# Kernel optimization log

Hardware: AMD Instinct MI355X
Metric: run time of the kernel (lower is better)

Reference implementation:

```python
import jax, jax.numpy as jnp
import numpy as np

B, S, E, H, NE, K = 4, 1024, 1024, 16, 8, 2
DFF = 4 * E
DH = E // H
EPS = 1e-5


def _ln(x, g, b):
    m = jnp.mean(x, axis=-1, keepdims=True)
    v = jnp.mean(jnp.square(x - m), axis=-1, keepdims=True)
    return (x - m) * jax.lax.rsqrt(v + EPS) * g + b


def setup_inputs() -> dict:
    key = jax.random.key(0)
    ks = jax.random.split(key, 20)
    n = lambda k, sh, s: (jax.random.normal(k, sh, jnp.float32) * s)
    return {
        'x': n(ks[0], (B, S, E), 1.0),
        'ln1_g': jnp.ones((E,), jnp.float32), 'ln1_b': jnp.zeros((E,), jnp.float32),
        'wq': n(ks[1], (E, E), 0.02), 'bq': jnp.zeros((E,), jnp.float32),
        'wk': n(ks[2], (E, E), 0.02), 'bk': jnp.zeros((E,), jnp.float32),
        'wv': n(ks[3], (E, E), 0.02), 'bv': jnp.zeros((E,), jnp.float32),
        'wo': n(ks[4], (E, E), 0.02), 'bo': jnp.zeros((E,), jnp.float32),
        'ln2_g': jnp.ones((E,), jnp.float32), 'ln2_b': jnp.zeros((E,), jnp.float32),
        'sw1': n(ks[5], (E, DFF), 0.02), 'sb1': jnp.zeros((DFF,), jnp.float32),
        'sw2': n(ks[6], (DFF, E), 0.02), 'sb2': jnp.zeros((E,), jnp.float32),
        'ew1': n(ks[7], (NE, E, DFF), 0.02), 'eb1': jnp.zeros((NE, DFF), jnp.float32),
        'ew2': n(ks[8], (NE, DFF, E), 0.02), 'eb2': jnp.zeros((NE, E), jnp.float32),
        'w_gate': n(ks[9], (E, NE), 1.0),
    }


def reference(x, ln1_g, ln1_b, wq, bq, wk, bk, wv, bv, wo, bo,
              ln2_g, ln2_b, sw1, sb1, sw2, sb2, ew1, eb1, ew2, eb2, w_gate):
    # --- self-attention sublayer (eval: no dropout) ---
    res1 = x
    h = _ln(x, ln1_g, ln1_b)
    q = (h @ wq + bq).reshape(B, S, H, DH)
    k = (h @ wk + bk).reshape(B, S, H, DH)
    v = (h @ wv + bv).reshape(B, S, H, DH)
    scores = jnp.einsum('bqhd,bkhd->bhqk', q, k) / jnp.sqrt(jnp.float32(DH))
    attn = jax.nn.softmax(scores, axis=-1)
    ctx = jnp.einsum('bhqk,bkhd->bqhd', attn, v).reshape(B, S, E)
    x = res1 + (ctx @ wo + bo)

    # --- MoE sublayer ---
    res2 = x
    h2 = _ln(x, ln2_g, ln2_b)
    shared = jax.nn.gelu(h2 @ sw1 + sb1, approximate=False) @ sw2 + sb2

    # router (eval: clean logits, no noise)
    logits = h2 @ w_gate                                  # (B,S,NE)
    top_vals, top_idx = jax.lax.top_k(logits, K)          # (B,S,K)
    top_gates = jax.nn.softmax(top_vals, axis=-1)
    onehot = jax.nn.one_hot(top_idx, NE, dtype=x.dtype)   # (B,S,K,NE)
    gates = jnp.einsum('bsk,bske->bse', top_gates, onehot)
    probs = jax.nn.softmax(logits, axis=-1).reshape(-1, NE)
    P = probs.mean(0)
    f = (gates > 0).astype(x.dtype).reshape(-1, NE).mean(0)
    aux_loss = NE * jnp.sum(P * f)

    # dense all-expert compute, gated combine (matches original math)
    eh = jax.nn.gelu(jnp.einsum('bse,neh->bnsh', h2, ew1) + eb1[None, :, None, :],
                     approximate=False)
    eo = jnp.einsum('bnsh,nhe->bnse', eh, ew2) + eb2[None, :, None, :]
    expert_out = jnp.einsum('bnse,bsn->bse', eo, gates)

    return res2 + shared + expert_out, aux_loss
```

## Files before the change

kernel.cpp:

```cpp
#include <hip/hip_runtime.h>
#include <stdint.h>

#define B_    4
#define S_    1024
#define E_    1024
#define H_    16
#define NE_   8
#define DFF_  4096
#define NT_   4096
#define QS_   3072
#define ROWCAP_ 9216

typedef unsigned short u16;
typedef short bf16x8 __attribute__((ext_vector_type(8)));
typedef float f32x4 __attribute__((ext_vector_type(4)));

__device__ __forceinline__ float bf2f(u16 u){ unsigned v = ((unsigned)u) << 16; return __builtin_bit_cast(float, v); }
__device__ __forceinline__ u16 f2bf(float f){ unsigned x = __builtin_bit_cast(unsigned, f); return (u16)((x + 0x7FFFu + ((x >> 16) & 1u)) >> 16); }
__device__ __forceinline__ float gelu_f(float x){ return 0.5f * x * (1.f + erff(x * 0.70710678118f)); }

__device__ __forceinline__ void gl_lds16(const u16* g, u16* l){
  __builtin_amdgcn_global_load_lds((__attribute__((address_space(1))) void*)(const_cast<u16*>(g)),
                                   (__attribute__((address_space(3))) void*)(l), 16, 0, 0);
}

__launch_bounds__(256)
__global__ void ln_kernel(const float* __restrict__ x, const float* __restrict__ g,
                          const float* __restrict__ be, u16* __restrict__ out)
{
  const int row = blockIdx.x;
  const float4 v = ((const float4*)(x + (size_t)row * E_))[threadIdx.x];
  float s = v.x + v.y + v.z + v.w;
  #pragma unroll
  for(int mm = 32; mm >= 1; mm >>= 1) s += __shfl_xor(s, mm);
  __shared__ float red[8];
  const int wid = threadIdx.x >> 6;
  if((threadIdx.x & 63) == 0) red[wid] = s;
  __syncthreads();
  const float mean = (red[0] + red[1] + red[2] + red[3]) * (1.0f / E_);
  const float d0 = v.x - mean, d1 = v.y - mean, d2 = v.z - mean, d3 = v.w - mean;
  float q2 = d0*d0 + d1*d1 + d2*d2 + d3*d3;
  #pragma unroll
  for(int mm = 32; mm >= 1; mm >>= 1) q2 += __shfl_xor(q2, mm);
  if((threadIdx.x & 63) == 0) red[4 + wid] = q2;
  __syncthreads();
  const float var = (red[4] + red[5] + red[6] + red[7]) * (1.0f / E_);
  const float rs = rsqrtf(var + 1e-5f);
  const float4 gg = ((const float4*)g)[threadIdx.x];
  const float4 bb = ((const float4*)be)[threadIdx.x];
  ushort4 o;
  o.x = f2bf(d0 * rs * gg.x + bb.x);
  o.y = f2bf(d1 * rs * gg.y + bb.y);
  o.z = f2bf(d2 * rs * gg.z + bb.z);
  o.w = f2bf(d3 * rs * gg.w + bb.w);
  ((ushort4*)(out + (size_t)row * E_))[threadIdx.x] = o;
}

__launch_bounds__(256)
__global__ void transpose_kernel(const float* __restrict__ W, u16* __restrict__ WT, int K, int N)
{
  __shared__ __align__(16) u16 t[64][72];
  const size_t zo = (size_t)blockIdx.z * K * N;
  const int k0 = blockIdx.x * 64, n0 = blockIdx.y * 64;
  const int tid = threadIdx.x;
  const int kr = tid >> 2;
  const int nc = (tid & 3) * 4;
  #pragma unroll
  for(int p = 0; p < 4; p++){
    float4 v = *(const float4*)(W + zo + (size_t)(k0 + kr) * N + n0 + nc + p * 16);
    t[nc + p*16 + 0][kr] = f2bf(v.x);
    t[nc + p*16 + 1][kr] = f2bf(v.y);
    t[nc + p*16 + 2][kr] = f2bf(v.z);
    t[nc + p*16 + 3][kr] = f2bf(v.w);
  }
  __syncthreads();
  const int nr = tid >> 3;
  const int kg = (tid & 7) * 8;
  #pragma unroll
  for(int p = 0; p < 2; p++){
    const int nn = nr + p * 32;
    unsigned u0 = t[nn][kg+0], u1 = t[nn][kg+1], u2 = t[nn][kg+2], u3 = t[nn][kg+3];
    unsigned u4 = t[nn][kg+4], u5 = t[nn][kg+5], u6 = t[nn][kg+6], u7 = t[nn][kg+7];
    uint4 o;
    o.x = u0 | (u1 << 16); o.y = u2 | (u3 << 16); o.z = u4 | (u5 << 16); o.w = u6 | (u7 << 16);
    *(uint4*)(WT + zo + (size_t)(n0 + nn) * K + k0 + kg) = o;
  }
}

__global__ void bcat_kernel(const float* __restrict__ bq, const float* __restrict__ bk,
                            const float* __restrict__ bv, float* __restrict__ bcat)
{
  const int i = blockIdx.x * 256 + threadIdx.x;
  if(i < 1024) bcat[i] = bq[i];
  else if(i < 2048) bcat[i] = bk[i - 1024];
  else if(i < 3072) bcat[i] = bv[i - 2048];
}

template<int MODE>
__launch_bounds__(256)
__global__ void gemm_kernel(const u16* __restrict__ A, const u16* __restrict__ Bt,
                            int N, int Kd, const float* __restrict__ bias,
                            u16* __restrict__ outB)
{
  __shared__ __align__(16) u16 As0[4096], Bs0[4096], As1[4096], Bs1[4096];
  const int tid = threadIdx.x, lane = tid & 63, wid = tid >> 6;
  const int wm = wid >> 1, wn = wid & 1;
  const int tm = blockIdx.y * 128, tn = blockIdx.x * 128;

  const f32x4 zero = {0.f, 0.f, 0.f, 0.f};
  f32x4 acc[4][4];
  #pragma unroll
  for(int m = 0; m < 4; m++)
    #pragma unroll
    for(int n = 0; n < 4; n++) acc[m][n] = zero;

  const u16* gA0 = A  + (size_t)(tm + wid*32 + (lane >> 2)) * Kd + ((lane & 3) << 3);
  const u16* gA1 = gA0 + (size_t)16 * Kd;
  const u16* gB0 = Bt + (size_t)(tn + wid*32 + (lane >> 2)) * Kd + ((lane & 3) << 3);
  const u16* gB1 = gB0 + (size_t)16 * Kd;
  u16* lA0 = As0 + wid*1024; u16* lA1 = lA0 + 512;
  u16* lB0 = Bs0 + wid*1024; u16* lB1 = lB0 + 512;
  u16* lA0b = As1 + wid*1024; u16* lA1b = lA0b + 512;
  u16* lB0b = Bs1 + wid*1024; u16* lB1b = lB0b + 512;

  for(int k0 = 0; k0 < Kd; k0 += 64){
    __syncthreads();
    gl_lds16(gA0 + k0, lA0);  gl_lds16(gA1 + k0, lA1);
    gl_lds16(gB0 + k0, lB0);  gl_lds16(gB1 + k0, lB1);
    gl_lds16(gA0 + k0+32, lA0b); gl_lds16(gA1 + k0+32, lA1b);
    gl_lds16(gB0 + k0+32, lB0b); gl_lds16(gB1 + k0+32, lB1b);
    __syncthreads();
    bf16x8 aF[4], bF[4];
    #pragma unroll
    for(int m = 0; m < 4; m++) aF[m] = *(const bf16x8*)(As0 + (wm*64 + m*16 + (lane & 15)) * 32 + ((lane >> 4) << 3));
    #pragma unroll
    for(int n = 0; n < 4; n++) bF[n] = *(const bf16x8*)(Bs0 + (wn*64 + n*16 + (lane & 15)) * 32 + ((lane >> 4) << 3));
    #pragma unroll
    for(int m = 0; m < 4; m++)
      #pragma unroll
      for(int n = 0; n < 4; n++)
        acc[m][n] = __builtin_amdgcn_mfma_f32_16x16x32_bf16(aF[m], bF[n], acc[m][n], 0, 0, 0);
    #pragma unroll
    for(int m = 0; m < 4; m++) aF[m] = *(const bf16x8*)(As1 + (wm*64 + m*16 + (lane & 15)) * 32 + ((lane >> 4) << 3));
    #pragma unroll
    for(int n = 0; n < 4; n++) bF[n] = *(const bf16x8*)(Bs1 + (wn*64 + n*16 + (lane & 15)) * 32 + ((lane >> 4) << 3));
    #pragma unroll
    for(int m = 0; m < 4; m++)
      #pragma unroll
      for(int n = 0; n < 4; n++)
        acc[m][n] = __builtin_amdgcn_mfma_f32_16x16x32_bf16(aF[m], bF[n], acc[m][n], 0, 0, 0);
  }

  #pragma unroll
  for(int m = 0; m < 4; m++){
    const int row = tm + wm*64 + m*16 + ((lane >> 4) << 2);
    #pragma unroll
    for(int n = 0; n < 4; n++){
      const int col = tn + wn*64 + n*16 + (lane & 15);
      const float bc = bias[col];
      #pragma unroll
      for(int r = 0; r < 4; r++){
        const float v = acc[m][n][r] + bc;
        const size_t idx = (size_t)(row + r) * N + col;
        if constexpr(MODE == 0) outB[idx] = f2bf(v);
        else outB[idx] = f2bf(gelu_f(v));
      }
    }
  }
}

template<int MODE>
__launch_bounds__(256)
__global__ void gemm64_kernel(const u16* __restrict__ A, const u16* __restrict__ Bt,
                              int N, int Kd, const float* __restrict__ bias,
                              float* __restrict__ outF, const float* __restrict__ resid)
{
  __shared__ __align__(16) u16 As0[2048], As1[2048], Bs0[4096], Bs1[4096];
  const int tid = threadIdx.x, lane = tid & 63, wid = tid >> 6;
  const int wm = wid >> 1, wn = wid & 1;
  const int tm = blockIdx.y * 64, tn = blockIdx.x * 128;

  const f32x4 zero = {0.f, 0.f, 0.f, 0.f};
  f32x4 acc[2][4];
  #pragma unroll
  for(int m = 0; m < 2; m++)
    #pragma unroll
    for(int n = 0; n < 4; n++) acc[m][n] = zero;

  const u16* gA = A + (size_t)(tm + wid*16 + (lane >> 2)) * Kd + ((lane & 3) << 3);
  const u16* gB0 = Bt + (size_t)(tn + wid*32 + (lane >> 2)) * Kd + ((lane & 3) << 3);
  const u16* gB1 = gB0 + (size_t)16 * Kd;
  u16* lA  = As0 + wid*512;  u16* lAb = As1 + wid*512;
  u16* lB0 = Bs0 + wid*1024; u16* lB1 = lB0 + 512;
  u16* lB0b = Bs1 + wid*1024; u16* lB1b = lB0b + 512;

  for(int k0 = 0; k0 < Kd; k0 += 64){
    __syncthreads();
    gl_lds16(gA + k0, lA);
    gl_lds16(gB0 + k0, lB0); gl_lds16(gB1 + k0, lB1);
    gl_lds16(gA + k0+32, lAb);
    gl_lds16(gB0 + k0+32, lB0b); gl_lds16(gB1 + k0+32, lB1b);
    __syncthreads();
    bf16x8 aF[2], bF[4];
    #pragma unroll
    for(int m = 0; m < 2; m++) aF[m] = *(const bf16x8*)(As0 + (wm*32 + m*16 + (lane & 15)) * 32 + ((lane >> 4) << 3));
    #pragma unroll
    for(int n = 0; n < 4; n++) bF[n] = *(const bf16x8*)(Bs0 + (wn*64 + n*16 + (lane & 15)) * 32 + ((lane >> 4) << 3));
    #pragma unroll
    for(int m = 0; m < 2; m++)
      #pragma unroll
      for(int n = 0; n < 4; n++)
        acc[m][n] = __builtin_amdgcn_mfma_f32_16x16x32_bf16(aF[m], bF[n], acc[m][n], 0, 0, 0);
    #pragma unroll
    for(int m = 0; m < 2; m++) aF[m] = *(const bf16x8*)(As1 + (wm*32 + m*16 + (lane & 15)) * 32 + ((lane >> 4) << 3));
    #pragma unroll
    for(int n = 0; n < 4; n++) bF[n] = *(const bf16x8*)(Bs1 + (wn*64 + n*16 + (lane & 15)) * 32 + ((lane >> 4) << 3));
    #pragma unroll
    for(int m = 0; m < 2; m++)
      #pragma unroll
      for(int n = 0; n < 4; n++)
        acc[m][n] = __builtin_amdgcn_mfma_f32_16x16x32_bf16(aF[m], bF[n], acc[m][n], 0, 0, 0);
  }

  #pragma unroll
  for(int m = 0; m < 2; m++){
    const int row = tm + wm*32 + m*16 + ((lane >> 4) << 2);
    #pragma unroll
    for(int n = 0; n < 4; n++){
      const int col = tn + wn*64 + n*16 + (lane & 15);
      const float bc = bias[col];
      #pragma unroll
      for(int r = 0; r < 4; r++){
        const float v = acc[m][n][r] + bc;
        const size_t idx = (size_t)(row + r) * N + col;
        if constexpr(MODE == 2) outF[idx] = resid[idx] + v;
        else outF[idx] += v;
      }
    }
  }
// ... 4 lines not shown
{
  __shared__ __align__(16) u16 Ks[64 * 64];
  __shared__ __align__(16) u16 Vt[64 * 72];
  __shared__ __align__(16) u16 Ps[64 * 72];
  const int tid = threadIdx.x, lane = tid & 63, wid = tid >> 6;
  const int bh = blockIdx.y, bb = bh >> 4, hh = bh & 15;
  const int q0 = blockIdx.x * 64;
  const size_t tok0 = (size_t)bb * S_;
  const int hcol = hh * 64;

  bf16x8 aQ0, aQ1;
  {
    const u16* qp = qkv + (tok0 + q0 + wid*16 + (lane & 15)) * QS_ + hcol + ((lane >> 4) << 3);
    aQ0 = *(const bf16x8*)qp;
    aQ1 = *(const bf16x8*)(qp + 32);
  }
  const f32x4 zero = {0.f, 0.f, 0.f, 0.f};
  f32x4 accO[4]; float mrow[4], lrow[4];
  #pragma unroll
  for(int n = 0; n < 4; n++) accO[n] = zero;
  #pragma unroll
  for(int r = 0; r < 4; r++){ mrow[r] = -1e30f; lrow[r] = 0.f; }
  const float sc = 0.125f * 1.44269504f;

  for(int kv0 = 0; kv0 < S_; kv0 += 64){
    __syncthreads();
    {
      const u16* gp = qkv + (tok0 + kv0 + wid*16 + (lane >> 3)) * QS_ + 1024 + hcol + ((lane & 7) << 3);
      gl_lds16(gp, Ks + (wid*16) * 64);
      gl_lds16(gp + (size_t)8 * QS_, Ks + (wid*16 + 8) * 64);
    }
    {
      #pragma unroll
      for(int i = 0; i < 2; i++){
        const int tok = (tid >> 3) + i * 32;
        const int d0 = (tid & 7) << 3;
        bf16x8 vv = *(const bf16x8*)(qkv + (tok0 + kv0 + tok) * QS_ + 2048 + hcol + d0);
        #pragma unroll
        for(int j = 0; j < 8; j++) Vt[(d0 + j) * 72 + tok] = (u16)vv[j];
      }
    }
    __syncthreads();
    f32x4 sf[4];
    #pragma unroll
    for(int n = 0; n < 4; n++){
      bf16x8 b0 = *(const bf16x8*)(Ks + (n*16 + (lane & 15)) * 64 + ((lane >> 4) << 3));
      bf16x8 b1 = *(const bf16x8*)(Ks + (n*16 + (lane & 15)) * 64 + 32 + ((lane >> 4) << 3));
      f32x4 t = zero;
      t = __builtin_amdgcn_mfma_f32_16x16x32_bf16(aQ0, b0, t, 0, 0, 0);
      t = __builtin_amdgcn_mfma_f32_16x16x32_bf16(aQ1, b1, t, 0, 0, 0);
      sf[n] = t;
    }
    #pragma unroll
    for(int r = 0; r < 4; r++){
      const float s0 = sf[0][r]*sc, s1 = sf[1][r]*sc, s2 = sf[2][r]*sc, s3 = sf[3][r]*sc;
      float mx = fmaxf(fmaxf(s0, s1), fmaxf(s2, s3));
      #pragma unroll
      for(int mm = 1; mm < 16; mm <<= 1) mx = fmaxf(mx, __shfl_xor(mx, mm));
      const float mnew = fmaxf(mrow[r], mx);
      const float resc = exp2f(mrow[r] - mnew);
      mrow[r] = mnew;
      const float p0 = exp2f(s0 - mnew), p1 = exp2f(s1 - mnew);
      const float p2 = exp2f(s2 - mnew), p3 = exp2f(s3 - mnew);
      float ps = p0 + p1 + p2 + p3;
      #pragma unroll
      for(int mm = 1; mm < 16; mm <<= 1) ps += __shfl_xor(ps, mm);
      lrow[r] = lrow[r] * resc + ps;
      #pragma unroll
      for(int n = 0; n < 4; n++) accO[n][r] *= resc;
      const int prow = wid*16 + ((lane >> 4) << 2) + r;
// ... 54 lines not shown
    float mx = lg[0];
    #pragma unroll
    for(int e = 1; e < 8; e++) mx = fmaxf(mx, lg[e]);
    float se = 0.f, ex[8];
    #pragma unroll
    for(int e = 0; e < 8; e++){ ex[e] = expf(lg[e] - mx); se += ex[e]; }
    const float inv = 1.f / se;
    float* pr = probs + (size_t)tok * 8;
    #pragma unroll
    for(int e = 0; e < 8; e++) pr[e] = ex[e] * inv;
    int i1 = 0; float v1 = lg[0];
    #pragma unroll
    for(int e = 1; e < 8; e++) if(lg[e] > v1){ v1 = lg[e]; i1 = e; }
    int i2 = -1; float v2 = -3.4e38f;
    #pragma unroll
    for(int e = 0; e < 8; e++) if(e != i1 && lg[e] > v2){ v2 = lg[e]; i2 = e; }
    const float t = expf(v2 - v1);
    tkidx[tok*2] = i1; tkidx[tok*2+1] = i2;
    tkgate[tok*2] = 1.f / (1.f + t); tkgate[tok*2+1] = t / (1.f + t);
    atomicAdd(&counts[i1], 1); atomicAdd(&counts[i2], 1);
  }
}

__global__ void init_kernel(int* __restrict__ counts, int* __restrict__ rowlist)
{
  const int t = blockIdx.x * 256 + threadIdx.x;
  if(t < 16) counts[t] = 0;
  if(t < ROWCAP_) rowlist[t] = -1;
}

__global__ void scan_kernel(const int* __restrict__ counts, int* __restrict__ aoff, int* __restrict__ cursor)
{
  if(threadIdx.x == 0){
    int o = 0;
    for(int e = 0; e < 8; e++){
      aoff[e] = o; cursor[e] = o;
      o += ((counts[e] + 127) >> 7) << 7;
    }
    aoff[8] = o;
  }
}

__global__ void build_kernel(const int* __restrict__ tkidx, const float* __restrict__ tkgate,
                             int* __restrict__ cursor, int* __restrict__ rowlist, float* __restrict__ rowgate)
{
  const int t = blockIdx.x * 256 + threadIdx.x;
  if(t >= NT_) return;
  #pragma unroll
  for(int kk = 0; kk < 2; kk++){
    const int e = tkidx[t*2 + kk];
    const int pos = atomicAdd(&cursor[e], 1);
    rowlist[pos] = t; rowgate[pos] = tkgate[t*2 + kk];
  }
}

__launch_bounds__(256)
__global__ void egemm1_kernel(const u16* __restrict__ Ah2, const u16* __restrict__ ewT,
                              const float* __restrict__ eb1,
                              const int* __restrict__ rowlist, const int* __restrict__ aoff,
                              u16* __restrict__ ehid)
{
  const int rowTile = blockIdx.y * 128;
  if(rowTile >= aoff[8]) return;
  int e = 0;
  #pragma unroll
  for(int i = 1; i < 8; i++) if(rowTile >= aoff[i]) e = i;
  __shared__ __align__(16) u16 As0[4096], Bs0[4096], As1[4096], Bs1[4096];
  const int tid = threadIdx.x, lane = tid & 63, wid = tid >> 6;
  const int wm = wid >> 1, wn = wid & 1;
  const int tn = blockIdx.x * 128;
  const u16* Bt = ewT + (size_t)e * DFF_ * E_;

  const int r0 = rowTile + wid*32 + (lane >> 2);
  int t0 = rowlist[r0];      if(t0 < 0) t0 = 0;
  int t1 = rowlist[r0 + 16]; if(t1 < 0) t1 = 0;
  const u16* gA0 = Ah2 + (size_t)t0 * E_ + ((lane & 3) << 3);
  const u16* gA1 = Ah2 + (size_t)t1 * E_ + ((lane & 3) << 3);
  const u16* gB0 = Bt + (size_t)(tn + wid*32 + (lane >> 2)) * E_ + ((lane & 3) << 3);
  const u16* gB1 = gB0 + (size_t)16 * E_;
  u16* lA0 = As0 + wid*1024; u16* lA1 = lA0 + 512;
  u16* lB0 = Bs0 + wid*1024; u16* lB1 = lB0 + 512;
  u16* lA0b = As1 + wid*1024; u16* lA1b = lA0b + 512;
  u16* lB0b = Bs1 + wid*1024; u16* lB1b = lB0b + 512;

  const f32x4 zero = {0.f,0.f,0.f,0.f};
  f32x4 acc[4][4];
  #pragma unroll
  for(int m = 0; m < 4; m++)
    #pragma unroll
    for(int n = 0; n < 4; n++) acc[m][n] = zero;

  for(int k0 = 0; k0 < E_; k0 += 64){
    __syncthreads();
    gl_lds16(gA0 + k0, lA0);  gl_lds16(gA1 + k0, lA1);
    gl_lds16(gB0 + k0, lB0);  gl_lds16(gB1 + k0, lB1);
    gl_lds16(gA0 + k0+32, lA0b); gl_lds16(gA1 + k0+32, lA1b);
    gl_lds16(gB0 + k0+32, lB0b); gl_lds16(gB1 + k0+32, lB1b);
    __syncthreads();
    bf16x8 aF[4], bF[4];
    #pragma unroll
    for(int m = 0; m < 4; m++) aF[m] = *(const bf16x8*)(As0 + (wm*64 + m*16 + (lane & 15)) * 32 + ((lane >> 4) << 3));
    #pragma unroll
    for(int n = 0; n < 4; n++) bF[n] = *(const bf16x8*)(Bs0 + (wn*64 + n*16 + (lane & 15)) * 32 + ((lane >> 4) << 3));
    #pragma unroll
    for(int m = 0; m < 4; m++)
      #pragma unroll
      for(int n = 0; n < 4; n++)
        acc[m][n] = __builtin_amdgcn_mfma_f32_16x16x32_bf16(aF[m], bF[n], acc[m][n], 0, 0, 0);
    #pragma unroll
    for(int m = 0; m < 4; m++) aF[m] = *(const bf16x8*)(As1 + (wm*64 + m*16 + (lane & 15)) * 32 + ((lane >> 4) << 3));
    #pragma unroll
    for(int n = 0; n < 4; n++) bF[n] = *(const bf16x8*)(Bs1 + (wn*64 + n*16 + (lane & 15)) * 32 + ((lane >> 4) << 3));
    #pragma unroll
    for(int m = 0; m < 4; m++)
      #pragma unroll
      for(int n = 0; n < 4; n++)
        acc[m][n] = __builtin_amdgcn_mfma_f32_16x16x32_bf16(aF[m], bF[n], acc[m][n], 0, 0, 0);
  }
  #pragma unroll
  for(int m = 0; m < 4; m++){
    const int row = rowTile + wm*64 + m*16 + ((lane >> 4) << 2);
    #pragma unroll
    for(int n = 0; n < 4; n++){
      const int col = tn + wn*64 + n*16 + (lane & 15);
      const float bc = eb1[e * DFF_ + col];
      #pragma unroll
      for(int r = 0; r < 4; r++)
        ehid[(size_t)(row + r) * DFF_ + col] = f2bf(gelu_f(acc[m][n][r] + bc));
    }
  }
}

__launch_bounds__(256)
__global__ void egemm2_kernel(const u16* __restrict__ ehid, const u16* __restrict__ ewT2,
                              const float* __restrict__ eb2,
                              const int* __restrict__ rowlist, const float* __restrict__ rowgate,
                              const int* __restrict__ aoff, float* __restrict__ outF)
{
  const int rowTile = blockIdx.y * 64;
  if(rowTile >= aoff[8]) return;
  int e = 0;
  #pragma unroll
  for(int i = 1; i < 8; i++) if(rowTile >= aoff[i]) e = i;
  __shared__ __align__(16) u16 As0[2048], As1[2048], Bs0[4096], Bs1[4096];
  const int tid = threadIdx.x, lane = tid & 63, wid = tid >> 6;
  const int wm = wid >> 1, wn = wid & 1;
  const int tn = blockIdx.x * 128;
  const u16* Bt = ewT2 + (size_t)e * E_ * DFF_;

  const u16* gA = ehid + (size_t)(rowTile + wid*16 + (lane >> 2)) * DFF_ + ((lane & 3) << 3);
  const u16* gB0 = Bt + (size_t)(tn + wid*32 + (lane >> 2)) * DFF_ + ((lane & 3) << 3);
  const u16* gB1 = gB0 + (size_t)16 * DFF_;
  u16* lA  = As0 + wid*512;  u16* lAb = As1 + wid*512;
  u16* lB0 = Bs0 + wid*1024; u16* lB1 = lB0 + 512;
  u16* lB0b = Bs1 + wid*1024; u16* lB1b = lB0b + 512;

  const f32x4 zero = {0.f,0.f,0.f,0.f};
  f32x4 acc[2][4];
  #pragma unroll
  for(int m = 0; m < 2; m++)
    #pragma unroll
    for(int n = 0; n < 4; n++) acc[m][n] = zero;

  for(int k0 = 0; k0 < DFF_; k0 += 64){
    __syncthreads();
    gl_lds16(gA + k0, lA);
    gl_lds16(gB0 + k0, lB0); gl_lds16(gB1 + k0, lB1);
    gl_lds16(gA + k0+32, lAb);
    gl_lds16(gB0 + k0+32, lB0b); gl_lds16(gB1 + k0+32, lB1b);
    __syncthreads();
    bf16x8 aF[2], bF[4];
    #pragma unroll
    for(int m = 0; m < 2; m++) aF[m] = *(const bf16x8*)(As0 + (wm*32 + m*16 + (lane & 15)) * 32 + ((lane >> 4) << 3));
    #pragma unroll
    for(int n = 0; n < 4; n++) bF[n] = *(const bf16x8*)(Bs0 + (wn*64 + n*16 + (lane & 15)) * 32 + ((lane >> 4) << 3));
    #pragma unroll
    for(int m = 0; m < 2; m++)
      #pragma unroll
      for(int n = 0; n < 4; n++)
        acc[m][n] = __builtin_amdgcn_mfma_f32_16x16x32_bf16(aF[m], bF[n], acc[m][n], 0, 0, 0);
    #pragma unroll
    for(int m = 0; m < 2; m++) aF[m] = *(const bf16x8*)(As1 + (wm*32 + m*16 + (lane & 15)) * 32 + ((lane >> 4) << 3));
    #pragma unroll
    for(int n = 0; n < 4; n++) bF[n] = *(const bf16x8*)(Bs1 + (wn*64 + n*16 + (lane & 15)) * 32 + ((lane >> 4) << 3));
    #pragma unroll
    for(int m = 0; m < 2; m++)
      #pragma unroll
      for(int n = 0; n < 4; n++)
        acc[m][n] = __builtin_amdgcn_mfma_f32_16x16x32_bf16(aF[m], bF[n], acc[m][n], 0, 0, 0);
  }
  #pragma unroll
  for(int m = 0; m < 2; m++){
    const int row = rowTile + wm*32 + m*16 + ((lane >> 4) << 2);
    #pragma unroll
    for(int r = 0; r < 4; r++){
      const int rr = row + r;
      const int tok = rowlist[rr];
      if(tok < 0) continue;
      const float g = rowgate[rr];
      #pragma unroll
      for(int n = 0; n < 4; n++){
        const int col = tn + wn*64 + n*16 + (lane & 15);
        atomicAdd(&outF[(size_t)tok * E_ + col], g * (acc[m][n][r] + eb2[e * E_ + col]));
      }
    }
  }
}

__launch_bounds__(256)
__global__ void aux_kernel(const float* __restrict__ probs, const int* __restrict__ counts,
                           float* __restrict__ outaux)
{
  float a[8];
  #pragma unroll
  for(int e = 0; e < 8; e++) a[e] = 0.f;
  for(int t = threadIdx.x; t < NT_; t += 256){
    const float* p = probs + (size_t)t * 8;
    #pragma unroll
    for(int e = 0; e < 8; e++) a[e] += p[e];
  }
  #pragma unroll
  for(int mm = 1; mm < 64; mm <<= 1)
    #pragma unroll
    for(int e = 0; e < 8; e++) a[e] += __shfl_xor(a[e], mm);
  __shared__ float part[4][8];
  const int wid = threadIdx.x >> 6;
  if((threadIdx.x & 63) == 0)
    for(int e = 0; e < 8; e++) part[wid][e] = a[e];
  __syncthreads();
  if(threadIdx.x == 0){
    float aux = 0.f;
    for(int e = 0; e < 8; e++){
      const float P = (part[0][e] + part[1][e] + part[2][e] + part[3][e]) / (float)NT_;
      const float f = (float)counts[e] / (float)NT_;
      aux += P * f;
    }
    outaux[0] = (float)NE_ * aux;
  }
}

extern "C" void kernel_launch(void* const* d_in, const int* in_sizes, int n_in,
                              void* d_out, int out_size, void* d_ws, size_t ws_size,
                              hipStream_t stream)
{
  (void)in_sizes; (void)n_in; (void)out_size; (void)ws_size;
  const float* x    = (const float*)d_in[0];
  const float* ln1g = (const float*)d_in[1];
  const float* ln1b = (const float*)d_in[2];
  const float* wq   = (const float*)d_in[3];
  const float* bq   = (const float*)d_in[4];
  const float* wk   = (const float*)d_in[5];
  const float* bk   = (const float*)d_in[6];
  const float* wv   = (const float*)d_in[7];
  const float* bv   = (const float*)d_in[8];
  const float* wo   = (const float*)d_in[9];
  const float* bo   = (const float*)d_in[10];
  const float* ln2g = (const float*)d_in[11];
  const float* ln2b = (const float*)d_in[12];
  const float* sw1  = (const float*)d_in[13];
  const float* sb1  = (const float*)d_in[14];
  const float* sw2  = (const float*)d_in[15];
  const float* sb2  = (const float*)d_in[16];
  const float* ew1  = (const float*)d_in[17];
  const float* eb1  = (const float*)d_in[18];
  const float* ew2  = (const float*)d_in[19];
  const float* eb2  = (const float*)d_in[20];
  const float* wgate= (const float*)d_in[21];
  float* out = (float*)d_out;
  char* ws = (char*)d_ws;

  const size_t MB = 1024ull * 1024ull;
  u16* h     = (u16*)(ws + 0);
  u16* h2    = (u16*)(ws + 8*MB);
  u16* wT    = (u16*)(ws + 16*MB);
  char* rt   = ws + 24*MB;
  float* probs   = (float*)(rt);
  float* tkgate  = (float*)(rt + 128*1024);
  int*   tkidx   = (int*)  (rt + 160*1024);
  int*   counts  = (int*)  (rt + 192*1024);
  int*   aoff    = (int*)  (rt + 192*1024 + 64);
  int*   cursor  = (int*)  (rt + 192*1024 + 128);
  int*   rowlist = (int*)  (rt + 256*1024);
  float* rowgate = (float*)(rt + 296*1024);
  float* bcat    = (float*)(rt + 512*1024);
  u16* qkvb  = (u16*)(ws + 32*MB);
  u16* ctx   = (u16*)(ws + 56*MB);
  u16* hidS  = (u16*)(ws + 64*MB);
  u16* ewT   = (u16*)(ws + 32*MB);
  u16* ehid  = (u16*)(ws + 96*MB);

  ln_kernel<<<NT_, 256, 0, stream>>>(x, ln1g, ln1b, h);
  bcat_kernel<<<12, 256, 0, stream>>>(bq, bk, bv, bcat);
  transpose_kernel<<<dim3(16,16,1), 256, 0, stream>>>(wq, wT,                 E_, E_);
  transpose_kernel<<<dim3(16,16,1), 256, 0, stream>>>(wk, wT + 1024*1024,     E_, E_);
  transpose_kernel<<<dim3(16,16,1), 256, 0, stream>>>(wv, wT + 2*1024*1024,   E_, E_);
  gemm_kernel<0><<<dim3(24,32), 256, 0, stream>>>(h, wT, QS_, E_, bcat, qkvb);
  attn_kernel<<<dim3(16,64), 256, 0, stream>>>(qkvb, ctx);
  transpose_kernel<<<dim3(16,16,1), 256, 0, stream>>>(wo, wT, E_, E_);
  gemm64_kernel<2><<<dim3(8,64), 256, 0, stream>>>(ctx, wT, E_, E_, bo, out, x);

  ln_kernel<<<NT_, 256, 0, stream>>>(out, ln2g, ln2b, h2);
  transpose_kernel<<<dim3(16,64,1), 256, 0, stream>>>(sw1, wT, E_, DFF_);
  gemm_kernel<1><<<dim3(32,32), 256, 0, stream>>>(h2, wT, DFF_, E_, sb1, hidS);
  transpose_kernel<<<dim3(64,16,1), 256, 0, stream>>>(sw2, wT, DFF_, E_);
  gemm64_kernel<3><<<dim3(8,64), 256, 0, stream>>>(hidS, wT, E_, DFF_, sb2, out, nullptr);

  init_kernel<<<36, 256, 0, stream>>>(counts, rowlist);
  router_kernel<<<1024, 256, 0, stream>>>(h2, wgate, probs, tkgate, tkidx, counts);
  scan_kernel<<<1, 64, 0, stream>>>(counts, aoff, cursor);
  build_kernel<<<16, 256, 0, stream>>>(tkidx, tkgate, cursor, rowlist, rowgate);

  transpose_kernel<<<dim3(16,64,8), 256, 0, stream>>>(ew1, ewT, E_, DFF_);
  egemm1_kernel<<<dim3(32,72), 256, 0, stream>>>(h2, ewT, eb1, rowlist, aoff, ehid);
  transpose_kernel<<<dim3(64,16,8), 256, 0, stream>>>(ew2, ewT, DFF_, E_);
  egemm2_kernel<<<dim3(8,144), 256, 0, stream>>>(ehid, ewT, eb2, rowlist, rowgate, aoff, out);

  aux_kernel<<<1, 256, 0, stream>>>(probs, counts, out + (size_t)NT_ * E_);
}
```

Baseline: 858.4 us.

## Fold shared FFN into grouped MoE GEMMs, swizzle LDS, batch transposes and prep

Treats the shared FFN as a ninth expert whose routed rows are all tokens with gate 1, so the shared and expert up/down projections run in the same grouped GEMM launches. This path is used when the workspace is large enough, with a fallback to the old schedule otherwise. It also XOR-swizzles the LDS layouts in all GEMM and attention kernels to cut bank conflicts, and merges the weight transposes and the bias/init kernels into fewer launches. The cost is a larger workspace and atomic accumulation of the shared output into the result, which may change float summation order.

```diff
diff --git a/kernel.cpp b/kernel.cpp
--- a/kernel.cpp
+++ b/kernel.cpp
@@ -9,7 +9,7 @@
 #define DFF_  4096
 #define NT_   4096
 #define QS_   3072
-#define ROWCAP_ 9216
+#define ROWCAP9_ 13440
 
 typedef unsigned short u16;
 typedef short bf16x8 __attribute__((ext_vector_type(8)));
@@ -23,6 +23,9 @@
   __builtin_amdgcn_global_load_lds((__attribute__((address_space(1))) void*)(const_cast<u16*>(g)),
                                    (__attribute__((address_space(3))) void*)(l), 16, 0, 0);
 }
+
+#define KSW32(l)   ((((l) & 3) ^ (((l) >> 3) & 3)) << 3)
+#define FRAGOFF(l) (((l) & 15) * 32 + (((((l) >> 4) ^ (((l) >> 1) & 3))) << 3))
 
 __launch_bounds__(256)
 __global__ void ln_kernel(const float* __restrict__ x, const float* __restrict__ g,
@@ -56,18 +59,16 @@
   ((ushort4*)(out + (size_t)row * E_))[threadIdx.x] = o;
 }
 
-__launch_bounds__(256)
-__global__ void transpose_kernel(const float* __restrict__ W, u16* __restrict__ WT, int K, int N)
+__device__ __forceinline__ void transpose_body(const float* __restrict__ W, u16* __restrict__ WT, int K, int N)
 {
   __shared__ __align__(16) u16 t[64][72];
-  const size_t zo = (size_t)blockIdx.z * K * N;
   const int k0 = blockIdx.x * 64, n0 = blockIdx.y * 64;
   const int tid = threadIdx.x;
   const int kr = tid >> 2;
   const int nc = (tid & 3) * 4;
   #pragma unroll
   for(int p = 0; p < 4; p++){
-    float4 v = *(const float4*)(W + zo + (size_t)(k0 + kr) * N + n0 + nc + p * 16);
+    float4 v = *(const float4*)(W + (size_t)(k0 + kr) * N + n0 + nc + p * 16);
     t[nc + p*16 + 0][kr] = f2bf(v.x);
     t[nc + p*16 + 1][kr] = f2bf(v.y);
     t[nc + p*16 + 2][kr] = f2bf(v.z);
@@ -83,17 +84,46 @@
     unsigned u4 = t[nn][kg+4], u5 = t[nn][kg+5], u6 = t[nn][kg+6], u7 = t[nn][kg+7];
     uint4 o;
     o.x = u0 | (u1 << 16); o.y = u2 | (u3 << 16); o.z = u4 | (u5 << 16); o.w = u6 | (u7 << 16);
-    *(uint4*)(WT + zo + (size_t)(n0 + nn) * K + k0 + kg) = o;
-  }
-}
-
-__global__ void bcat_kernel(const float* __restrict__ bq, const float* __restrict__ bk,
-                            const float* __restrict__ bv, float* __restrict__ bcat)
-{
-  const int i = blockIdx.x * 256 + threadIdx.x;
-  if(i < 1024) bcat[i] = bq[i];
-  else if(i < 2048) bcat[i] = bk[i - 1024];
-  else if(i < 3072) bcat[i] = bv[i - 2048];
+    *(uint4*)(WT + (size_t)(n0 + nn) * K + k0 + kg) = o;
+  }
+}
+
+__launch_bounds__(256)
+__global__ void transpose_kernel(const float* __restrict__ W, u16* __restrict__ WT, int K, int N)
+{ transpose_body(W, WT, K, N); }
+
+__launch_bounds__(256)
+__global__ void transpose4_kernel(const float* wq, const float* wk, const float* wv, const float* wo,
+                                  u16* __restrict__ WT)
+{
+  const float* W = (blockIdx.z == 0) ? wq : (blockIdx.z == 1) ? wk : (blockIdx.z == 2) ? wv : wo;
+  transpose_body(W, WT + (size_t)blockIdx.z * E_ * E_, E_, E_);
+}
+
+__launch_bounds__(256)
+__global__ void transpose9_kernel(const float* __restrict__ ew, const float* __restrict__ sw,
+                                  u16* __restrict__ WT, int K, int N)
+{
+  const float* W = (blockIdx.z < 8) ? (ew + (size_t)blockIdx.z * K * N) : sw;
+  transpose_body(W, WT + (size_t)blockIdx.z * K * N, K, N);
+}
+
+__global__ void prep_kernel(const float* __restrict__ bq, const float* __restrict__ bk,
+                            const float* __restrict__ bv, float* __restrict__ bcat,
+                            int* __restrict__ counts, int* __restrict__ rowlist,
+                            const float* __restrict__ eb1, const float* __restrict__ sb1,
+                            float* __restrict__ b9up,
+                            const float* __restrict__ eb2, const float* __restrict__ sb2,
+                            float* __restrict__ b9dn)
+{
+  const int stride = gridDim.x * 256;
+  for(int i = blockIdx.x * 256 + threadIdx.x; i < 9 * DFF_; i += stride){
+    b9up[i] = (i < 8 * DFF_) ? eb1[i] : sb1[i - 8 * DFF_];
+    if(i < 9 * E_)   b9dn[i] = (i < 8 * E_) ? eb2[i] : sb2[i - 8 * E_];
+    if(i < QS_)      bcat[i] = (i < E_) ? bq[i] : (i < 2*E_) ? bk[i - E_] : bv[i - 2*E_];
+    if(i < 16)       counts[i] = 0;
+    if(i < ROWCAP9_) rowlist[i] = -1;
+  }
 }
 
 template<int MODE>
@@ -114,14 +144,17 @@
     #pragma unroll
     for(int n = 0; n < 4; n++) acc[m][n] = zero;
 
-  const u16* gA0 = A  + (size_t)(tm + wid*32 + (lane >> 2)) * Kd + ((lane & 3) << 3);
+  const int ksw = KSW32(lane);
+  const u16* gA0 = A  + (size_t)(tm + wid*32 + (lane >> 2)) * Kd + ksw;
   const u16* gA1 = gA0 + (size_t)16 * Kd;
-  const u16* gB0 = Bt + (size_t)(tn + wid*32 + (lane >> 2)) * Kd + ((lane & 3) << 3);
+  const u16* gB0 = Bt + (size_t)(tn + wid*32 + (lane >> 2)) * Kd + ksw;
   const u16* gB1 = gB0 + (size_t)16 * Kd;
   u16* lA0 = As0 + wid*1024; u16* lA1 = lA0 + 512;
   u16* lB0 = Bs0 + wid*1024; u16* lB1 = lB0 + 512;
   u16* lA0b = As1 + wid*1024; u16* lA1b = lA0b + 512;
   u16* lB0b = Bs1 + wid*1024; u16* lB1b = lB0b + 512;
+  const int fo = FRAGOFF(lane);
+  const int fA = wm * 2048, fB = wn * 2048;
 
   for(int k0 = 0; k0 < Kd; k0 += 64){
     __syncthreads();
@@ -132,18 +165,18 @@
     __syncthreads();
     bf16x8 aF[4], bF[4];
     #pragma unroll
-    for(int m = 0; m < 4; m++) aF[m] = *(const bf16x8*)(As0 + (wm*64 + m*16 + (lane & 15)) * 32 + ((lane >> 4) << 3));
-    #pragma unroll
-    for(int n = 0; n < 4; n++) bF[n] = *(const bf16x8*)(Bs0 + (wn*64 + n*16 + (lane & 15)) * 32 + ((lane >> 4) << 3));
+    for(int m = 0; m < 4; m++) aF[m] = *(const bf16x8*)(As0 + fA + m*512 + fo);
+    #pragma unroll
+    for(int n = 0; n < 4; n++) bF[n] = *(const bf16x8*)(Bs0 + fB + n*512 + fo);
     #pragma unroll
     for(int m = 0; m < 4; m++)
       #pragma unroll
       for(int n = 0; n < 4; n++)
         acc[m][n] = __builtin_amdgcn_mfma_f32_16x16x32_bf16(aF[m], bF[n], acc[m][n], 0, 0, 0);
     #pragma unroll
-    for(int m = 0; m < 4; m++) aF[m] = *(const bf16x8*)(As1 + (wm*64 + m*16 + (lane & 15)) * 32 + ((lane >> 4) << 3));
-    #pragma unroll
-    for(int n = 0; n < 4; n++) bF[n] = *(const bf16x8*)(Bs1 + (wn*64 + n*16 + (lane & 15)) * 32 + ((lane >> 4) << 3));
+    for(int m = 0; m < 4; m++) aF[m] = *(const bf16x8*)(As1 + fA + m*512 + fo);
+    #pragma unroll
+    for(int n = 0; n < 4; n++) bF[n] = *(const bf16x8*)(Bs1 + fB + n*512 + fo);
     #pragma unroll
     for(int m = 0; m < 4; m++)
       #pragma unroll
@@ -187,12 +220,15 @@
     #pragma unroll
     for(int n = 0; n < 4; n++) acc[m][n] = zero;
 
-  const u16* gA = A + (size_t)(tm + wid*16 + (lane >> 2)) * Kd + ((lane & 3) << 3);
-  const u16* gB0 = Bt + (size_t)(tn + wid*32 + (lane >> 2)) * Kd + ((lane & 3) << 3);
+  const int ksw = KSW32(lane);
+  const u16* gA = A + (size_t)(tm + wid*16 + (lane >> 2)) * Kd + ksw;
+  const u16* gB0 = Bt + (size_t)(tn + wid*32 + (lane >> 2)) * Kd + ksw;
   const u16* gB1 = gB0 + (size_t)16 * Kd;
   u16* lA  = As0 + wid*512;  u16* lAb = As1 + wid*512;
   u16* lB0 = Bs0 + wid*1024; u16* lB1 = lB0 + 512;
   u16* lB0b = Bs1 + wid*1024; u16* lB1b = lB0b + 512;
+  const int fo = FRAGOFF(lane);
+  const int fA = wm * 1024, fB = wn * 2048;
 
   for(int k0 = 0; k0 < Kd; k0 += 64){
     __syncthreads();
@@ -203,18 +239,18 @@
     __syncthreads();
     bf16x8 aF[2], bF[4];
     #pragma unroll
-    for(int m = 0; m < 2; m++) aF[m] = *(const bf16x8*)(As0 + (wm*32 + m*16 + (lane & 15)) * 32 + ((lane >> 4) << 3));
-    #pragma unroll
-    for(int n = 0; n < 4; n++) bF[n] = *(const bf16x8*)(Bs0 + (wn*64 + n*16 + (lane & 15)) * 32 + ((lane >> 4) << 3));
+    for(int m = 0; m < 2; m++) aF[m] = *(const bf16x8*)(As0 + fA + m*512 + fo);
+    #pragma unroll
+    for(int n = 0; n < 4; n++) bF[n] = *(const bf16x8*)(Bs0 + fB + n*512 + fo);
     #pragma unroll
     for(int m = 0; m < 2; m++)
       #pragma unroll
       for(int n = 0; n < 4; n++)
         acc[m][n] = __builtin_amdgcn_mfma_f32_16x16x32_bf16(aF[m], bF[n], acc[m][n], 0, 0, 0);
     #pragma unroll
-    for(int m = 0; m < 2; m++) aF[m] = *(const bf16x8*)(As1 + (wm*32 + m*16 + (lane & 15)) * 32 + ((lane >> 4) << 3));
-    #pragma unroll
-    for(int n = 0; n < 4; n++) bF[n] = *(const bf16x8*)(Bs1 + (wn*64 + n*16 + (lane & 15)) * 32 + ((lane >> 4) << 3));
+    for(int m = 0; m < 2; m++) aF[m] = *(const bf16x8*)(As1 + fA + m*512 + fo);
+    #pragma unroll
+    for(int n = 0; n < 4; n++) bF[n] = *(const bf16x8*)(Bs1 + fB + n*512 + fo);
     #pragma unroll
     for(int m = 0; m < 2; m++)
       #pragma unroll
@@ -265,11 +301,12 @@
   #pragma unroll
   for(int r = 0; r < 4; r++){ mrow[r] = -1e30f; lrow[r] = 0.f; }
   const float sc = 0.125f * 1.44269504f;
+  const int ksw8 = (((lane & 7) ^ ((lane >> 3) & 7)) << 3);
 
   for(int kv0 = 0; kv0 < S_; kv0 += 64){
     __syncthreads();
     {
-      const u16* gp = qkv + (tok0 + kv0 + wid*16 + (lane >> 3)) * QS_ + 1024 + hcol + ((lane & 7) << 3);
+      const u16* gp = qkv + (tok0 + kv0 + wid*16 + (lane >> 3)) * QS_ + 1024 + hcol + ksw8;
       gl_lds16(gp, Ks + (wid*16) * 64);
       gl_lds16(gp + (size_t)8 * QS_, Ks + (wid*16 + 8) * 64);
     }
@@ -287,8 +324,9 @@
     f32x4 sf[4];
     #pragma unroll
     for(int n = 0; n < 4; n++){
-      bf16x8 b0 = *(const bf16x8*)(Ks + (n*16 + (lane & 15)) * 64 + ((lane >> 4) << 3));
-      bf16x8 b1 = *(const bf16x8*)(Ks + (n*16 + (lane & 15)) * 64 + 32 + ((lane >> 4) << 3));
+      const int rb = n*16 + (lane & 15);
+      bf16x8 b0 = *(const bf16x8*)(Ks + rb*64 + ((((lane >> 4)    ) ^ (lane & 7)) << 3));
+      bf16x8 b1 = *(const bf16x8*)(Ks + rb*64 + ((((lane >> 4) + 4) ^ (lane & 7)) << 3));
       f32x4 t = zero;
       t = __builtin_amdgcn_mfma_f32_16x16x32_bf16(aQ0, b0, t, 0, 0, 0);
       t = __builtin_amdgcn_mfma_f32_16x16x32_bf16(aQ1, b1, t, 0, 0, 0);
@@ -389,14 +427,8 @@
   }
 }
 
-__global__ void init_kernel(int* __restrict__ counts, int* __restrict__ rowlist)
-{
-  const int t = blockIdx.x * 256 + threadIdx.x;
-  if(t < 16) counts[t] = 0;
-  if(t < ROWCAP_) rowlist[t] = -1;
-}
-
-__global__ void scan_kernel(const int* __restrict__ counts, int* __restrict__ aoff, int* __restrict__ cursor)
+__global__ void scan_kernel(const int* __restrict__ counts, int* __restrict__ aoff,
+                            int* __restrict__ cursor, int addShared)
 {
   if(threadIdx.x == 0){
     int o = 0;
@@ -405,11 +437,13 @@
       o += ((counts[e] + 127) >> 7) << 7;
     }
     aoff[8] = o;
+    aoff[9] = o + (addShared ? NT_ : 0);
   }
 }
 
 __global__ void build_kernel(const int* __restrict__ tkidx, const float* __restrict__ tkgate,
-                             int* __restrict__ cursor, int* __restrict__ rowlist, float* __restrict__ rowgate)
+                             int* __restrict__ cursor, int* __restrict__ rowlist,
+                             float* __restrict__ rowgate, const int* __restrict__ aoff, int addShared)
 {
   const int t = blockIdx.x * 256 + threadIdx.x;
   if(t >= NT_) return;
@@ -419,36 +453,43 @@
     const int pos = atomicAdd(&cursor[e], 1);
     rowlist[pos] = t; rowgate[pos] = tkgate[t*2 + kk];
   }
-}
-
-__launch_bounds__(256)
-__global__ void egemm1_kernel(const u16* __restrict__ Ah2, const u16* __restrict__ ewT,
-                              const float* __restrict__ eb1,
-                              const int* __restrict__ rowlist, const int* __restrict__ aoff,
-                              u16* __restrict__ ehid)
+  if(addShared){
+    const int base = aoff[8];
+    rowlist[base + t] = t; rowgate[base + t] = 1.f;
+  }
+}
+
+__launch_bounds__(256)
+__global__ void upmoe_kernel(const u16* __restrict__ Ah2, const u16* __restrict__ W1T,
+                             const float* __restrict__ b9up,
+                             const int* __restrict__ rowlist, const int* __restrict__ aoff,
+                             u16* __restrict__ ehid)
 {
   const int rowTile = blockIdx.y * 128;
-  if(rowTile >= aoff[8]) return;
+  if(rowTile >= aoff[9]) return;
   int e = 0;
   #pragma unroll
-  for(int i = 1; i < 8; i++) if(rowTile >= aoff[i]) e = i;
+  for(int i = 1; i <= 8; i++) if(rowTile >= aoff[i]) e = i;
   __shared__ __align__(16) u16 As0[4096], Bs0[4096], As1[4096], Bs1[4096];
   const int tid = threadIdx.x, lane = tid & 63, wid = tid >> 6;
   const int wm = wid >> 1, wn = wid & 1;
   const int tn = blockIdx.x * 128;
-  const u16* Bt = ewT + (size_t)e * DFF_ * E_;
+  const u16* Bt = W1T + (size_t)e * DFF_ * E_;
 
   const int r0 = rowTile + wid*32 + (lane >> 2);
   int t0 = rowlist[r0];      if(t0 < 0) t0 = 0;
   int t1 = rowlist[r0 + 16]; if(t1 < 0) t1 = 0;
-  const u16* gA0 = Ah2 + (size_t)t0 * E_ + ((lane & 3) << 3);
-  const u16* gA1 = Ah2 + (size_t)t1 * E_ + ((lane & 3) << 3);
-  const u16* gB0 = Bt + (size_t)(tn + wid*32 + (lane >> 2)) * E_ + ((lane & 3) << 3);
+  const int ksw = KSW32(lane);
+  const u16* gA0 = Ah2 + (size_t)t0 * E_ + ksw;
+  const u16* gA1 = Ah2 + (size_t)t1 * E_ + ksw;
+  const u16* gB0 = Bt + (size_t)(tn + wid*32 + (lane >> 2)) * E_ + ksw;
   const u16* gB1 = gB0 + (size_t)16 * E_;
   u16* lA0 = As0 + wid*1024; u16* lA1 = lA0 + 512;
   u16* lB0 = Bs0 + wid*1024; u16* lB1 = lB0 + 512;
   u16* lA0b = As1 + wid*1024; u16* lA1b = lA0b + 512;
   u16* lB0b = Bs1 + wid*1024; u16* lB1b = lB0b + 512;
+  const int fo = FRAGOFF(lane);
+  const int fA = wm * 2048, fB = wn * 2048;
 
   const f32x4 zero = {0.f,0.f,0.f,0.f};
   f32x4 acc[4][4];
@@ -466,18 +507,18 @@
     __syncthreads();
     bf16x8 aF[4], bF[4];
     #pragma unroll
-    for(int m = 0; m < 4; m++) aF[m] = *(const bf16x8*)(As0 + (wm*64 + m*16 + (lane & 15)) * 32 + ((lane >> 4) << 3));
-    #pragma unroll
-    for(int n = 0; n < 4; n++) bF[n] = *(const bf16x8*)(Bs0 + (wn*64 + n*16 + (lane & 15)) * 32 + ((lane >> 4) << 3));
+    for(int m = 0; m < 4; m++) aF[m] = *(const bf16x8*)(As0 + fA + m*512 + fo);
+    #pragma unroll
+    for(int n = 0; n < 4; n++) bF[n] = *(const bf16x8*)(Bs0 + fB + n*512 + fo);
     #pragma unroll
     for(int m = 0; m < 4; m++)
       #pragma unroll
       for(int n = 0; n < 4; n++)
         acc[m][n] = __builtin_amdgcn_mfma_f32_16x16x32_bf16(aF[m], bF[n], acc[m][n], 0, 0, 0);
     #pragma unroll
-    for(int m = 0; m < 4; m++) aF[m] = *(const bf16x8*)(As1 + (wm*64 + m*16 + (lane & 15)) * 32 + ((lane >> 4) << 3));
-    #pragma unroll
-    for(int n = 0; n < 4; n++) bF[n] = *(const bf16x8*)(Bs1 + (wn*64 + n*16 + (lane & 15)) * 32 + ((lane >> 4) << 3));
+    for(int m = 0; m < 4; m++) aF[m] = *(const bf16x8*)(As1 + fA + m*512 + fo);
+    #pragma unroll
+    for(int n = 0; n < 4; n++) bF[n] = *(const bf16x8*)(Bs1 + fB + n*512 + fo);
     #pragma unroll
     for(int m = 0; m < 4; m++)
       #pragma unroll
@@ -490,7 +531,7 @@
     #pragma unroll
     for(int n = 0; n < 4; n++){
       const int col = tn + wn*64 + n*16 + (lane & 15);
-      const float bc = eb1[e * DFF_ + col];
+      const float bc = b9up[e * DFF_ + col];
       #pragma unroll
       for(int r = 0; r < 4; r++)
         ehid[(size_t)(row + r) * DFF_ + col] = f2bf(gelu_f(acc[m][n][r] + bc));
@@ -499,28 +540,31 @@
 }
 
 __launch_bounds__(256)
-__global__ void egemm2_kernel(const u16* __restrict__ ehid, const u16* __restrict__ ewT2,
-                              const float* __restrict__ eb2,
-                              const int* __restrict__ rowlist, const float* __restrict__ rowgate,
-                              const int* __restrict__ aoff, float* __restrict__ outF)
+__global__ void downmoe_kernel(const u16* __restrict__ ehid, const u16* __restrict__ W2T,
+                               const float* __restrict__ b9dn,
+                               const int* __restrict__ rowlist, const float* __restrict__ rowgate,
+                               const int* __restrict__ aoff, float* __restrict__ outF)
 {
   const int rowTile = blockIdx.y * 64;
-  if(rowTile >= aoff[8]) return;
+  if(rowTile >= aoff[9]) return;
   int e = 0;
   #pragma unroll
-  for(int i = 1; i < 8; i++) if(rowTile >= aoff[i]) e = i;
+  for(int i = 1; i <= 8; i++) if(rowTile >= aoff[i]) e = i;
   __shared__ __align__(16) u16 As0[2048], As1[2048], Bs0[4096], Bs1[4096];
   const int tid = threadIdx.x, lane = tid & 63, wid = tid >> 6;
   const int wm = wid >> 1, wn = wid & 1;
   const int tn = blockIdx.x * 128;
-  const u16* Bt = ewT2 + (size_t)e * E_ * DFF_;
-
-  const u16* gA = ehid + (size_t)(rowTile + wid*16 + (lane >> 2)) * DFF_ + ((lane & 3) << 3);
-  const u16* gB0 = Bt + (size_t)(tn + wid*32 + (lane >> 2)) * DFF_ + ((lane & 3) << 3);
+  const u16* Bt = W2T + (size_t)e * E_ * DFF_;
+
+  const int ksw = KSW32(lane);
+  const u16* gA = ehid + (size_t)(rowTile + wid*16 + (lane >> 2)) * DFF_ + ksw;
+  const u16* gB0 = Bt + (size_t)(tn + wid*32 + (lane >> 2)) * DFF_ + ksw;
   const u16* gB1 = gB0 + (size_t)16 * DFF_;
   u16* lA  = As0 + wid*512;  u16* lAb = As1 + wid*512;
   u16* lB0 = Bs0 + wid*1024; u16* lB1 = lB0 + 512;
   u16* lB0b = Bs1 + wid*1024; u16* lB1b = lB0b + 512;
+  const int fo = FRAGOFF(lane);
+  const int fA = wm * 1024, fB = wn * 2048;
 
   const f32x4 zero = {0.f,0.f,0.f,0.f};
   f32x4 acc[2][4];
@@ -538,18 +582,18 @@
     __syncthreads();
     bf16x8 aF[2], bF[4];
     #pragma unroll
-    for(int m = 0; m < 2; m++) aF[m] = *(const bf16x8*)(As0 + (wm*32 + m*16 + (lane & 15)) * 32 + ((lane >> 4) << 3));
-    #pragma unroll
-    for(int n = 0; n < 4; n++) bF[n] = *(const bf16x8*)(Bs0 + (wn*64 + n*16 + (lane & 15)) * 32 + ((lane >> 4) << 3));
+    for(int m = 0; m < 2; m++) aF[m] = *(const bf16x8*)(As0 + fA + m*512 + fo);
+    #pragma unroll
+    for(int n = 0; n < 4; n++) bF[n] = *(const bf16x8*)(Bs0 + fB + n*512 + fo);
     #pragma unroll
     for(int m = 0; m < 2; m++)
       #pragma unroll
       for(int n = 0; n < 4; n++)
         acc[m][n] = __builtin_amdgcn_mfma_f32_16x16x32_bf16(aF[m], bF[n], acc[m][n], 0, 0, 0);
     #pragma unroll
-    for(int m = 0; m < 2; m++) aF[m] = *(const bf16x8*)(As1 + (wm*32 + m*16 + (lane & 15)) * 32 + ((lane >> 4) << 3));
-    #pragma unroll
-    for(int n = 0; n < 4; n++) bF[n] = *(const bf16x8*)(Bs1 + (wn*64 + n*16 + (lane & 15)) * 32 + ((lane >> 4) << 3));
+    for(int m = 0; m < 2; m++) aF[m] = *(const bf16x8*)(As1 + fA + m*512 + fo);
+    #pragma unroll
+    for(int n = 0; n < 4; n++) bF[n] = *(const bf16x8*)(Bs1 + fB + n*512 + fo);
     #pragma unroll
     for(int m = 0; m < 2; m++)
       #pragma unroll
@@ -568,7 +612,7 @@
       #pragma unroll
       for(int n = 0; n < 4; n++){
         const int col = tn + wn*64 + n*16 + (lane & 15);
-        atomicAdd(&outF[(size_t)tok * E_ + col], g * (acc[m][n][r] + eb2[e * E_ + col]));
+        atomicAdd(&outF[(size_t)tok * E_ + col], g * (acc[m][n][r] + b9dn[e * E_ + col]));
       }
     }
   }
@@ -610,7 +654,7 @@
                               void* d_out, int out_size, void* d_ws, size_t ws_size,
                               hipStream_t stream)
 {
-  (void)in_sizes; (void)n_in; (void)out_size; (void)ws_size;
+  (void)in_sizes; (void)n_in; (void)out_size;
   const float* x    = (const float*)d_in[0];
   const float* ln1g = (const float*)d_in[1];
   const float* ln1b = (const float*)d_in[2];
@@ -635,52 +679,76 @@
   const float* wgate= (const float*)d_in[21];
   float* out = (float*)d_out;
   char* ws = (char*)d_ws;
-
   const size_t MB = 1024ull * 1024ull;
-  u16* h     = (u16*)(ws + 0);
-  u16* h2    = (u16*)(ws + 8*MB);
-  u16* wT    = (u16*)(ws + 16*MB);
-  char* rt   = ws + 24*MB;
+  const bool big = (ws_size >= 194 * MB);
+
+  char* rt = big ? (ws + 192*MB) : (ws + 24*MB);
   float* probs   = (float*)(rt);
-  float* tkgate  = (float*)(rt + 128*1024);
-  int*   tkidx   = (int*)  (rt + 160*1024);
-  int*   counts  = (int*)  (rt + 192*1024);
-  int*   aoff    = (int*)  (rt + 192*1024 + 64);
-  int*   cursor  = (int*)  (rt + 192*1024 + 128);
-  int*   rowlist = (int*)  (rt + 256*1024);
-  float* rowgate = (float*)(rt + 296*1024);
-  float* bcat    = (float*)(rt + 512*1024);
-  u16* qkvb  = (u16*)(ws + 32*MB);
-  u16* ctx   = (u16*)(ws + 56*MB);
-  u16* hidS  = (u16*)(ws + 64*MB);
-  u16* ewT   = (u16*)(ws + 32*MB);
-  u16* ehid  = (u16*)(ws + 96*MB);
-
-  ln_kernel<<<NT_, 256, 0, stream>>>(x, ln1g, ln1b, h);
-  bcat_kernel<<<12, 256, 0, stream>>>(bq, bk, bv, bcat);
-  transpose_kernel<<<dim3(16,16,1), 256, 0, stream>>>(wq, wT,                 E_, E_);
-  transpose_kernel<<<dim3(16,16,1), 256, 0, stream>>>(wk, wT + 1024*1024,     E_, E_);
-  transpose_kernel<<<dim3(16,16,1), 256, 0, stream>>>(wv, wT + 2*1024*1024,   E_, E_);
-  gemm_kernel<0><<<dim3(24,32), 256, 0, stream>>>(h, wT, QS_, E_, bcat, qkvb);
-  attn_kernel<<<dim3(16,64), 256, 0, stream>>>(qkvb, ctx);
-  transpose_kernel<<<dim3(16,16,1), 256, 0, stream>>>(wo, wT, E_, E_);
-  gemm64_kernel<2><<<dim3(8,64), 256, 0, stream>>>(ctx, wT, E_, E_, bo, out, x);
-
-  ln_kernel<<<NT_, 256, 0, stream>>>(out, ln2g, ln2b, h2);
-  transpose_kernel<<<dim3(16,64,1), 256, 0, stream>>>(sw1, wT, E_, DFF_);
-  gemm_kernel<1><<<dim3(32,32), 256, 0, stream>>>(h2, wT, DFF_, E_, sb1, hidS);
-  transpose_kernel<<<dim3(64,16,1), 256, 0, stream>>>(sw2, wT, DFF_, E_);
-  gemm64_kernel<3><<<dim3(8,64), 256, 0, stream>>>(hidS, wT, E_, DFF_, sb2, out, nullptr);
-
-  init_kernel<<<36, 256, 0, stream>>>(counts, rowlist);
-  router_kernel<<<1024, 256, 0, stream>>>(h2, wgate, probs, tkgate, tkidx, counts);
-  scan_kernel<<<1, 64, 0, stream>>>(counts, aoff, cursor);
-  build_kernel<<<16, 256, 0, stream>>>(tkidx, tkgate, cursor, rowlist, rowgate);
-
-  transpose_kernel<<<dim3(16,64,8), 256, 0, stream>>>(ew1, ewT, E_, DFF_);
-  egemm1_kernel<<<dim3(32,72), 256, 0, stream>>>(h2, ewT, eb1, rowlist, aoff, ehid);
-  transpose_kernel<<<dim3(64,16,8), 256, 0, stream>>>(ew2, ewT, DFF_, E_);
-  egemm2_kernel<<<dim3(8,144), 256, 0, stream>>>(ehid, ewT, eb2, rowlist, rowgate, aoff, out);
-
-  aux_kernel<<<1, 256, 0, stream>>>(probs, counts, out + (size_t)NT_ * E_);
-}
+  float* tkgate  = (float*)(rt + 131072);
+  int*   tkidx   = (int*)  (rt + 163840);
+  int*   counts  = (int*)  (rt + 196608);
+  int*   aoff    = (int*)  (rt + 196672);
+  int*   cursor  = (int*)  (rt + 196736);
+  int*   rowlist = (int*)  (rt + 196800);
+  float* rowgate = (float*)(rt + 250560);
+  float* bcat    = (float*)(rt + 304320);
+  float* b9up    = (float*)(rt + 316608);
+  float* b9dn    = (float*)(rt + 464064);
+
+  if(big){
+    u16* h    = (u16*)(ws + 0);
+    u16* qkvb = (u16*)(ws + 8*MB);
+    u16* ctx  = (u16*)(ws + 32*MB);
+    u16* wT4  = (u16*)(ws + 40*MB);
+    u16* ehid = (u16*)(ws + 0);
+    u16* W1T  = (u16*)(ws + 112*MB);
+    u16* W2T  = W1T;
+    u16* h2   = (u16*)(ws + 184*MB);
+
+    prep_kernel<<<64, 256, 0, stream>>>(bq, bk, bv, bcat, counts, rowlist, eb1, sb1, b9up, eb2, sb2, b9dn);
+    transpose4_kernel<<<dim3(16,16,4), 256, 0, stream>>>(wq, wk, wv, wo, wT4);
+    transpose9_kernel<<<dim3(16,64,9), 256, 0, stream>>>(ew1, sw1, W1T, E_, DFF_);
+    ln_kernel<<<NT_, 256, 0, stream>>>(x, ln1g, ln1b, h);
+    gemm_kernel<0><<<dim3(24,32), 256, 0, stream>>>(h, wT4, QS_, E_, bcat, qkvb);
+    attn_kernel<<<dim3(16,64), 256, 0, stream>>>(qkvb, ctx);
+    gemm64_kernel<2><<<dim3(8,64), 256, 0, stream>>>(ctx, wT4 + 3u*1024*1024, E_, E_, bo, out, x);
+    ln_kernel<<<NT_, 256, 0, stream>>>(out, ln2g, ln2b, h2);
+    router_kernel<<<1024, 256, 0, stream>>>(h2, wgate, probs, tkgate, tkidx, counts);
+    scan_kernel<<<1, 64, 0, stream>>>(counts, aoff, cursor, 1);
+    build_kernel<<<16, 256, 0, stream>>>(tkidx, tkgate, cursor, rowlist, rowgate, aoff, 1);
+    upmoe_kernel<<<dim3(32,105), 256, 0, stream>>>(h2, W1T, b9up, rowlist, aoff, ehid);
+    transpose9_kernel<<<dim3(64,16,9), 256, 0, stream>>>(ew2, sw2, W2T, DFF_, E_);
+    downmoe_kernel<<<dim3(8,210), 256, 0, stream>>>(ehid, W2T, b9dn, rowlist, rowgate, aoff, out);
+    aux_kernel<<<1, 256, 0, stream>>>(probs, counts, out + (size_t)NT_ * E_);
+  } else {
+    u16* h    = (u16*)(ws + 0);
+    u16* h2   = (u16*)(ws + 8*MB);
+    u16* wT4  = (u16*)(ws + 16*MB);
+    u16* swT  = wT4;
+    u16* qkvb = (u16*)(ws + 32*MB);
+    u16* ctx  = (u16*)(ws + 56*MB);
+    u16* hidS = (u16*)(ws + 64*MB);
+    u16* ewT  = (u16*)(ws + 32*MB);
+    u16* ehid = (u16*)(ws + 96*MB);
+
+    prep_kernel<<<64, 256, 0, stream>>>(bq, bk, bv, bcat, counts, rowlist, eb1, sb1, b9up, eb2, sb2, b9dn);
+    transpose4_kernel<<<dim3(16,16,4), 256, 0, stream>>>(wq, wk, wv, wo, wT4);
+    ln_kernel<<<NT_, 256, 0, stream>>>(x, ln1g, ln1b, h);
+    gemm_kernel<0><<<dim3(24,32), 256, 0, stream>>>(h, wT4, QS_, E_, bcat, qkvb);
+    attn_kernel<<<dim3(16,64), 256, 0, stream>>>(qkvb, ctx);
+    gemm64_kernel<2><<<dim3(8,64), 256, 0, stream>>>(ctx, wT4 + 3u*1024*1024, E_, E_, bo, out, x);
+    ln_kernel<<<NT_, 256, 0, stream>>>(out, ln2g, ln2b, h2);
+    transpose_kernel<<<dim3(16,64), 256, 0, stream>>>(sw1, swT, E_, DFF_);
+    gemm_kernel<1><<<dim3(32,32), 256, 0, stream>>>(h2, swT, DFF_, E_, sb1, hidS);
+    transpose_kernel<<<dim3(64,16), 256, 0, stream>>>(sw2, swT, DFF_, E_);
+    gemm64_kernel<3><<<dim3(8,64), 256, 0, stream>>>(hidS, swT, E_, DFF_, sb2, out, nullptr);
+    router_kernel<<<1024, 256, 0, stream>>>(h2, wgate, probs, tkgate, tkidx, counts);
+    scan_kernel<<<1, 64, 0, stream>>>(counts, aoff, cursor, 0);
+    build_kernel<<<16, 256, 0, stream>>>(tkidx, tkgate, cursor, rowlist, rowgate, aoff, 0);
+    transpose9_kernel<<<dim3(16,64,8), 256, 0, stream>>>(ew1, sw1, ewT, E_, DFF_);
+    upmoe_kernel<<<dim3(32,105), 256, 0, stream>>>(h2, ewT, b9up, rowlist, aoff, ehid);
+    transpose9_kernel<<<dim3(64,16,8), 256, 0, stream>>>(ew2, sw2, ewT, DFF_, E_);
+    downmoe_kernel<<<dim3(8,210), 256, 0, stream>>>(ehid, ewT, b9dn, rowlist, rowgate, aoff, out);
+    aux_kernel<<<1, 256, 0, stream>>>(probs, counts, out + (size_t)NT_ * E_);
+  }
+}
```

After: 808.5 us. 1.06x faster.
